# Kernel tuning notes

Hardware: AMD Instinct MI355X
Metric: run time of the kernel (lower is better)

The kernel has to match this reference:

```python
import jax, jax.numpy as jnp
import numpy as np

HEADS = 4
DIM_HEAD = 32


def setup_inputs() -> dict:
    key = jax.random.key(0)
    k1, k2, k3, k4 = jax.random.split(key, 4)
    x = jax.random.normal(k1, (2, 64, 48, 48, 48), dtype=jnp.float32)
    # 1x1x1 conv weights collapse to plain channel-mixing matrices
    w_qkv = jax.random.normal(k2, (384, 64), dtype=jnp.float32) * 0.05  # [3*heads*dh, dim]
    w_out = jax.random.normal(k3, (64, 128), dtype=jnp.float32) * 0.05  # [dim, heads*dh]
    b_out = jax.random.normal(k4, (64,), dtype=jnp.float32) * 0.05
    return {"x": x, "w_qkv": w_qkv, "w_out": w_out, "b_out": b_out}


def reference(x, w_qkv, w_out, b_out):
    b, c, D, H, W = x.shape
    N = D * H * W
    x_flat = x.reshape(b, c, N)
    # 1x1 conv == channel matmul: [b, 3*heads*dh, N]
    qkv = jnp.einsum('oc,bcn->bon', w_qkv, x_flat)
    # channel order: (qkv, heads, dh)
    qkv = qkv.reshape(b, 3, HEADS, DIM_HEAD, N)
    q, k, v = qkv[:, 0], qkv[:, 1], qkv[:, 2]
    k = jax.nn.softmax(k, axis=-1)  # softmax over the token axis N
    context = jnp.einsum('bhdn,bhen->bhde', k, v)   # [b, h, dh, dh]
    out = jnp.einsum('bhde,bhdn->bhen', context, q)  # [b, h, dh, N]
    out = out.reshape(b, HEADS * DIM_HEAD, N)
    y = jnp.einsum('oc,bcn->bon', w_out, out) + b_out[None, :, None]
    return y.reshape(b, c, D, H, W)
```

## Files before the change

### kernel.cpp

```cpp
#include <hip/hip_runtime.h>


#define C_IN 64

typedef __attribute__((ext_vector_type(8))) short short8;
typedef __attribute__((ext_vector_type(4))) float f32x4;

static __device__ __forceinline__ unsigned short f2bf(float f) {
    union { float f; unsigned u; } x; x.f = f;
    return (unsigned short)((x.u + 0x7fffu + ((x.u >> 16) & 1u)) >> 16);
}

__global__ __launch_bounds__(256, 3)
void kv_ctx_fused(const float* __restrict__ x,
                  const float* __restrict__ w_qkv,
                  unsigned short* __restrict__ xT,
                  float* __restrict__ part,
                  int N, int nblk, int bbase)
{
    __shared__ __align__(16) unsigned short Xsb[64][68];
    __shared__ __align__(16) unsigned short Xbf[64][72];
    __shared__ __align__(16) unsigned short PVs[4 * 2 * 32 * 64];

    const int by  = blockIdx.y;
    const int b   = by + bbase;
    const int bx  = blockIdx.x;
    const int t   = threadIdx.x;
    const int w   = t >> 6;
    const int l   = t & 63;
    const int l15 = l & 15;
    const int lg  = l >> 4;

    const float* xb = x + (size_t)b * C_IN * N;
    const int n_blk = bx * 256;

    auto pv_ptr = [&](int wp, int row, int colbf) -> unsigned short* {
        int byte = ((wp * 32 + row) << 7) + (((colbf << 1)) ^ ((row & 7) << 4));
        return (unsigned short*)((char*)PVs + byte);
    };

    short8 Wf[4][2];
    #pragma unroll
    for (int nt = 0; nt < 4; ++nt) {
        const int row = (nt < 2) ? (128 + w * 32 + nt * 16 + l15)
                                 : (256 + w * 32 + (nt - 2) * 16 + l15);
        const float* wr = w_qkv + (size_t)row * C_IN;
        #pragma unroll
        for (int s = 0; s < 2; ++s) {
            #pragma unroll
            for (int j = 0; j < 8; ++j)
                Wf[nt][s][j] = (short)f2bf(wr[s * 32 + lg * 8 + j]);
        }
    }

    f32x4 acc2[2][2];
    #pragma unroll
    for (int dt = 0; dt < 2; ++dt)
        #pragma unroll
        for (int et = 0; et < 2; ++et)
            acc2[dt][et] = (f32x4){0.f, 0.f, 0.f, 0.f};
    float s_loc[2] = {0.f, 0.f};

    float4 ld0, ld1, ld2, ld3;

    #define ISSUE_LOADS(IT) {                                              \
        const int nb2 = n_blk + (IT) * 64;                                 \
        int slot, c, nq;                                                   \
        slot = 0 * 256 + t; c = slot >> 4; nq = slot & 15;                 \
        ld0 = *(const float4*)(xb + (size_t)c * N + nb2 + nq * 4);         \
        slot = 1 * 256 + t; c = slot >> 4; nq = slot & 15;                 \
        ld1 = *(const float4*)(xb + (size_t)c * N + nb2 + nq * 4);         \
        slot = 2 * 256 + t; c = slot >> 4; nq = slot & 15;                 \
        ld2 = *(const float4*)(xb + (size_t)c * N + nb2 + nq * 4);         \
        slot = 3 * 256 + t; c = slot >> 4; nq = slot & 15;                 \
        ld3 = *(const float4*)(xb + (size_t)c * N + nb2 + nq * 4);         \
    }
    #define STORE_XSB() {                                                  \
        float4 lds_[4] = {ld0, ld1, ld2, ld3};                             \
        _Pragma("unroll")                                                  \
        for (int i = 0; i < 4; ++i) {                                      \
            int slot = i * 256 + t;                                        \
            int c = slot >> 4, n4 = (slot & 15) * 4;                       \
            uint2 p;                                                       \
            p.x = (unsigned)f2bf(lds_[i].x) | ((unsigned)f2bf(lds_[i].y) << 16); \
            p.y = (unsigned)f2bf(lds_[i].z) | ((unsigned)f2bf(lds_[i].w) << 16); \
            *(uint2*)&Xsb[c][n4] = p;                                      \
        }                                                                  \
    }

    ISSUE_LOADS(0)
    STORE_XSB()
    __syncthreads();

    for (int it = 0; it < 4; ++it) {
        if (it < 3) ISSUE_LOADS(it + 1)

        {
            const int an = l;
            unsigned rowu[8];
            #pragma unroll
            for (int i = 0; i < 8; ++i) {
                unsigned lo = Xsb[w * 16 + 2 * i][an];
                unsigned hi = Xsb[w * 16 + 2 * i + 1][an];
                rowu[i] = lo | (hi << 16);
            }
            *(uint4*)&Xbf[an][w * 16]     = *(uint4*)&rowu[0];
            *(uint4*)&Xbf[an][w * 16 + 8] = *(uint4*)&rowu[4];
            unsigned short* dst = xT + ((size_t)by * N + n_blk + it * 64 + an) * 64 + w * 16;
            *(uint4*)(dst)     = *(uint4*)&rowu[0];
            *(uint4*)(dst + 8) = *(uint4*)&rowu[4];
        }
        __syncthreads();

        short8 Af[4][2];
        #pragma unroll
        for (int mt = 0; mt < 4; ++mt)
            #pragma unroll
            for (int s = 0; s < 2; ++s)
                Af[mt][s] = *(const short8*)&Xbf[mt * 16 + l15][s * 32 + lg * 8];

        #pragma unroll
        for (int mt = 0; mt < 4; ++mt) {
            #pragma unroll
            for (int nt = 0; nt < 4; ++nt) {
                f32x4 a = (f32x4){0.f, 0.f, 0.f, 0.f};
                a = __builtin_amdgcn_mfma_f32_16x16x32_bf16(Af[mt][0], Wf[nt][0], a, 0, 0, 0);
                a = __builtin_amdgcn_mfma_f32_16x16x32_bf16(Af[mt][1], Wf[nt][1], a, 0, 0, 0);
                const int nl = mt * 16 + lg * 4;
                if (nt < 2) {
                    float e0 = __expf(a[0]), e1 = __expf(a[1]);
                    float e2 = __expf(a[2]), e3 = __expf(a[3]);
                    s_loc[nt] += (e0 + e1) + (e2 + e3);
                    uint2 p;
                    p.x = (unsigned)f2bf(e0) | ((unsigned)f2bf(e1) << 16);
                    p.y = (unsigned)f2bf(e2) | ((unsigned)f2bf(e3) << 16);
                    *(uint2*)pv_ptr(w * 2, (nt & 1) * 16 + l15, nl) = p;
                } else {
                    uint2 p;
                    p.x = (unsigned)f2bf(a[0]) | ((unsigned)f2bf(a[1]) << 16);
                    p.y = (unsigned)f2bf(a[2]) | ((unsigned)f2bf(a[3]) << 16);
                    *(uint2*)pv_ptr(w * 2 + 1, (nt - 2) * 16 + l15, nl) = p;
                }
            }
        }

        #pragma unroll
        for (int ns = 0; ns < 2; ++ns) {
            short8 A2[2], B2[2];
            #pragma unroll
            for (int dt = 0; dt < 2; ++dt)
                A2[dt] = *(const short8*)pv_ptr(w * 2, dt * 16 + l15, ns * 32 + lg * 8);
            #pragma unroll
            for (int et = 0; et < 2; ++et)
                B2[et] = *(const short8*)pv_ptr(w * 2 + 1, et * 16 + l15, ns * 32 + lg * 8);
            #pragma unroll
            for (int dt = 0; dt < 2; ++dt)
                #pragma unroll
                for (int et = 0; et < 2; ++et)
                    acc2[dt][et] = __builtin_amdgcn_mfma_f32_16x16x32_bf16(
                        A2[dt], B2[et], acc2[dt][et], 0, 0, 0);
        }

        if (it < 3) STORE_XSB()
        __syncthreads();
    }
    #undef ISSUE_LOADS
    #undef STORE_XSB

    float* pb = part + ((size_t)b * nblk + bx) * 4224;
    #pragma unroll
    for (int dt = 0; dt < 2; ++dt)
        #pragma unroll
        for (int et = 0; et < 2; ++et)
            #pragma unroll
            for (int r = 0; r < 4; ++r)
                pb[(w * 32 + dt * 16 + lg * 4 + r) * 32 + et * 16 + l15] =
                    acc2[dt][et][r];

    #pragma unroll
    for (int nt = 0; nt < 2; ++nt) {
        float s = s_loc[nt];
        s += __shfl_xor(s, 16);
        s += __shfl_xor(s, 32);
        if (lg == 0)
            pb[4096 + w * 32 + nt * 16 + l15] = s;
    }
}

__global__ __launch_bounds__(256)
void reduce_kernel(const float* __restrict__ part,
                   float* __restrict__ part2,
                   int nblk)
{
    const int b  = blockIdx.z;
    const int cy = blockIdx.y;
    const int g  = blockIdx.x * 256 + threadIdx.x;
    if (g >= 4224) return;

    const int cnt = (nblk + 15) / 16;
    const int c0  = cy * cnt;
    const int c1  = (c0 + cnt < nblk) ? (c0 + cnt) : nblk;

    const float* pb = part + (size_t)b * nblk * 4224 + g;
    float a0 = 0.f, a1 = 0.f, a2 = 0.f, a3 = 0.f;
    int c = c0;
    for (; c + 4 <= c1; c += 4) {
        a0 += pb[(size_t)(c + 0) * 4224];
        a1 += pb[(size_t)(c + 1) * 4224];
        a2 += pb[(size_t)(c + 2) * 4224];
        a3 += pb[(size_t)(c + 3) * 4224];
    }
    for (; c < c1; ++c) a0 += pb[(size_t)c * 4224];
    part2[((size_t)b * 16 + cy) * 4224 + g] = (a0 + a1) + (a2 + a3);
}

__global__ __launch_bounds__(256)
void finalize_kernel(const float* __restrict__ part2,
                     const float* __restrict__ w_qkv,
                     const float* __restrict__ w_out,
                     unsigned short* __restrict__ wf_bf)
{
    const int b = blockIdx.y;
    const int s = blockIdx.x;
    const int t = threadIdx.x;

    __shared__ float Wq[128][64];
    __shared__ float Ctx[128][36];
    __shared__ float Tt[128][68];
    __shared__ float WoS[8][128];
    __shared__ float Sinv[128];

    #pragma unroll
    for (int i = 0; i < 8; ++i) {
        int idx = i * 1024 + t * 4;
        *(float4*)&Wq[idx >> 6][idx & 63] = *(const float4*)(w_qkv + idx);
    }
    {
        int idx = t * 4;
        int o = idx >> 7, he = idx & 127;
        *(float4*)&WoS[o][he] = *(const float4*)(w_out + (size_t)(s * 8 + o) * 128 + he);
    }
    if (t < 128) {
        float ssum = 0.f;
        #pragma unroll
        for (int rep = 0; rep < 16; ++rep)
            ssum += part2[((size_t)b * 16 + rep) * 4224 + 4096 + t];
        Sinv[t] = 1.0f / ssum;
    }
    float cacc[16];
    #pragma unroll
    for (int i = 0; i < 16; ++i) cacc[i] = 0.f;
    {
        const float* cb = part2 + (size_t)b * 16 * 4224;
        for (int rep = 0; rep < 16; ++rep) {
            #pragma unroll
            for (int i = 0; i < 16; ++i)
                cacc[i] += cb[(size_t)rep * 4224 + i * 256 + t];
        }
    }
    __syncthreads();

    #pragma unroll
    for (int i = 0; i < 16; ++i) {
        int idx = i * 256 + t;
        Ctx[idx >> 5][idx & 31] = cacc[i] * Sinv[idx >> 5];
    }
    __syncthreads();

    {
        const int he0 = (t >> 3) * 4;
        const int c0  = (t & 7) * 8;
        const int hh  = he0 >> 5;
        const int e0  = he0 & 31;
        float acc[4][8];
        #pragma unroll
        for (int j = 0; j < 4; ++j)
            #pragma unroll
            for (int k = 0; k < 8; ++k) acc[j][k] = 0.f;

        for (int d = 0; d < 32; ++d) {
            float4 cv = *(const float4*)&Ctx[hh * 32 + d][e0];
            float4 w0 = *(const float4*)&Wq[hh * 32 + d][c0];
            float4 w1 = *(const float4*)&Wq[hh * 32 + d][c0 + 4];
            float wv[8] = {w0.x, w0.y, w0.z, w0.w, w1.x, w1.y, w1.z, w1.w};
            float cvv[4] = {cv.x, cv.y, cv.z, cv.w};
            #pragma unroll
            for (int j = 0; j < 4; ++j)
                #pragma unroll
                for (int k = 0; k < 8; ++k)
                    acc[j][k] = fmaf(cvv[j], wv[k], acc[j][k]);
        }
        #pragma unroll
        for (int j = 0; j < 4; ++j) {
            *(float4*)&Tt[he0 + j][c0]     = make_float4(acc[j][0], acc[j][1], acc[j][2], acc[j][3]);
            *(float4*)&Tt[he0 + j][c0 + 4] = make_float4(acc[j][4], acc[j][5], acc[j][6], acc[j][7]);
        }
    }
    __syncthreads();

    {
        const int o = t >> 5;
        const int c = (t & 31) * 2;
        float a0 = 0.f, a1 = 0.f, b0 = 0.f, b1 = 0.f;
        #pragma unroll
        for (int he = 0; he < 128; he += 2) {
            float w0 = WoS[o][he], w1 = WoS[o][he + 1];
            float2 t0 = *(const float2*)&Tt[he][c];
            float2 t1 = *(const float2*)&Tt[he + 1][c];
            a0 = fmaf(w0, t0.x, a0); a1 = fmaf(w0, t0.y, a1);
            b0 = fmaf(w1, t1.x, b0); b1 = fmaf(w1, t1.y, b1);
        }
        unsigned short* dst = wf_bf + (size_t)b * 4096 + (size_t)(s * 8 + o) * 64 + c;
        dst[0] = f2bf(a0 + b0);
        dst[1] = f2bf(a1 + b1);
    }
}

__global__ __launch_bounds__(256)
void out_gemm_mfma(const unsigned short* __restrict__ xT,
                   const unsigned short* __restrict__ wf_bf,
                   const float* __restrict__ b_out,
                   float* __restrict__ y,
                   int N, int bbase)
{
    const int by  = blockIdx.y;
    const int b   = by + bbase;
    const int t   = threadIdx.x;
    const int w   = t >> 6;
    const int l   = t & 63;
    const int l15 = l & 15;
    const int lg  = l >> 4;
    const int nb  = blockIdx.x * 256 + w * 64;

    short8 Bf[4][2];
    const unsigned short* wb = wf_bf + (size_t)b * 4096;
    #pragma unroll
    for (int ot = 0; ot < 4; ++ot)
        #pragma unroll
        for (int s = 0; s < 2; ++s)
            Bf[ot][s] = *(const short8*)(wb + (size_t)(ot * 16 + l15) * 64
                                         + s * 32 + lg * 8);
    float bias[4];
    #pragma unroll
    for (int ot = 0; ot < 4; ++ot) bias[ot] = b_out[ot * 16 + l15];

    short8 Af[4][2];
    const unsigned short* xr = xT + ((size_t)by * N + nb) * 64;
    #pragma unroll
    for (int mt = 0; mt < 4; ++mt)
        #pragma unroll
        for (int s = 0; s < 2; ++s)
            Af[mt][s] = *(const short8*)(xr + (size_t)(mt * 16 + l15) * 64
                                         + s * 32 + lg * 8);

    float* yb = y + (size_t)b * C_IN * N;
    #pragma unroll
    for (int mt = 0; mt < 4; ++mt) {
        #pragma unroll
        for (int ot = 0; ot < 4; ++ot) {
            f32x4 a = (f32x4){0.f, 0.f, 0.f, 0.f};
            a = __builtin_amdgcn_mfma_f32_16x16x32_bf16(Af[mt][0], Bf[ot][0], a, 0, 0, 0);
            a = __builtin_amdgcn_mfma_f32_16x16x32_bf16(Af[mt][1], Bf[ot][1], a, 0, 0, 0);
            float4 v = make_float4(a[0] + bias[ot], a[1] + bias[ot],
                                   a[2] + bias[ot], a[3] + bias[ot]);
            *(float4*)(yb + (size_t)(ot * 16 + l15) * N + nb + mt * 16 + lg * 4) = v;
        }
    }
}

__global__ __launch_bounds__(256)
void transpose_kernel(const float* __restrict__ x,
                      unsigned short* __restrict__ xT,
                      int N, int bbase)
{
    __shared__ float Xs[64][65];
    const int b  = blockIdx.y + bbase;
    const int t  = threadIdx.x;
    const int n0 = blockIdx.x * 64;

    const float* xb = x + (size_t)b * C_IN * N;
    #pragma unroll
    for (int i = 0; i < 4; ++i) {
        int slot = i * 256 + t;
        int c = slot >> 4, nq = slot & 15;
        float4 v = *(const float4*)(xb + (size_t)c * N + n0 + nq * 4);
        Xs[c][nq * 4 + 0] = v.x; Xs[c][nq * 4 + 1] = v.y;
        Xs[c][nq * 4 + 2] = v.z; Xs[c][nq * 4 + 3] = v.w;
    }
    __syncthreads();

    const int n = t >> 2, q = t & 3;
    unsigned out[8];
    #pragma unroll
    for (int i = 0; i < 8; ++i) {
        float lo = Xs[q * 16 + 2 * i][n], hi = Xs[q * 16 + 2 * i + 1][n];
        out[i] = (unsigned)f2bf(lo) | ((unsigned)f2bf(hi) << 16);
    }
    unsigned short* dst = xT + ((size_t)blockIdx.y * N + n0 + n) * 64 + q * 16;
    *(uint4*)(dst)     = *(uint4*)&out[0];
    *(uint4*)(dst + 8) = *(uint4*)&out[4];
}

extern "C" void kernel_launch(void* const* d_in, const int* in_sizes, int n_in,
                              void* d_out, int out_size, void* d_ws, size_t ws_size,
                              hipStream_t stream)
{
    const float* x     = (const float*)d_in[0];
    const float* w_qkv = (const float*)d_in[1];
    const float* w_out = (const float*)d_in[2];
    const float* b_out = (const float*)d_in[3];
    float* y = (float*)d_out;

    const int B = 2;
    const int N = in_sizes[0] / (B * C_IN);
    const int nblk = N / 256;

    const size_t xT_batch = (size_t)N * 64 * 2;
    const size_t part_b   = (size_t)B * nblk * 4224 * 4;
    const size_t p2_b     = (size_t)B * 16 * 4224 * 4;
    const size_t wf_b     = (size_t)B * 4096 * 2;
    const bool   full     = ws_size >= (size_t)B * xT_batch + part_b + p2_b + wf_b;

    unsigned short* xT    = (unsigned short*)d_ws;
    char* p               = (char*)d_ws + (full ? B * xT_batch : xT_batch);
    float* part           = (float*)p;
    float* part2          = part + (size_t)B * nblk * 4224;
    unsigned short* wf_bf = (unsigned short*)(part2 + (size_t)B * 16 * 4224);

    if (full) {
        kv_ctx_fused<<<dim3(nblk, B), 256, 0, stream>>>(x, w_qkv, xT, part, N, nblk, 0);
        reduce_kernel<<<dim3(17, 16, B), 256, 0, stream>>>(part, part2, nblk);
        finalize_kernel<<<dim3(8, B), 256, 0, stream>>>(part2, w_qkv, w_out, wf_bf);
        out_gemm_mfma<<<dim3(nblk, B), 256, 0, stream>>>(xT, wf_bf, b_out, y, N, 0);
    } else {
        for (int b = 0; b < B; ++b)
            kv_ctx_fused<<<dim3(nblk, 1), 256, 0, stream>>>(x, w_qkv, xT, part, N, nblk, b);
        reduce_kernel<<<dim3(17, 16, B), 256, 0, stream>>>(part, part2, nblk);
        finalize_kernel<<<dim3(8, B), 256, 0, stream>>>(part2, w_qkv, w_out, wf_bf);
        for (int b = 0; b < B; ++b) {
            transpose_kernel<<<dim3(N / 64, 1), 256, 0, stream>>>(x, xT, N, b);
            out_gemm_mfma<<<dim3(nblk, 1), 256, 0, stream>>>(xT, wf_bf, b_out, y, N, b);
        }
    }
}
```

Before: 67.40 us.

## Fuse four kernels into one cooperative persistent kernel with grid syncs

Replaces the four-kernel pipeline (kv context, reduce, finalize, output GEMM) with a single cooperative kernel. Each block processes two 256-token units, and grid.sync separates the phases. This removes launch gaps and tail effects between the kernels. In exchange it adds three grid-wide barriers, idles most blocks during the small reduce and finalize phases, and relies on co-residency of 432 blocks. It falls back to the old multi-kernel path if cooperative launch is unavailable, and the low-workspace per-batch fallback is removed.

Result: no change. 67.59 us (+0.3%).

```diff
diff --git a/kernel.cpp b/kernel.cpp
--- a/kernel.cpp
+++ b/kernel.cpp
@@ -1,4 +1,7 @@
 #include <hip/hip_runtime.h>
+#include <hip/hip_cooperative_groups.h>
+
+namespace cg = cooperative_groups;
 
 
 #define C_IN 64
@@ -9,6 +12,352 @@
 static __device__ __forceinline__ unsigned short f2bf(float f) {
     union { float f; unsigned u; } x; x.f = f;
     return (unsigned short)((x.u + 0x7fffu + ((x.u >> 16) & 1u)) >> 16);
+}
+
+__global__ __launch_bounds__(256, 3)
+void mega_kernel(const float* __restrict__ x,
+                 const float* __restrict__ w_qkv,
+                 const float* __restrict__ w_out,
+                 const float* __restrict__ b_out,
+                 unsigned short* __restrict__ xT,
+                 float* __restrict__ part,
+                 float* __restrict__ part2,
+                 unsigned short* __restrict__ wf_bf,
+                 float* __restrict__ y,
+                 int N, int nblk)
+{
+    cg::grid_group grid = cg::this_grid();
+    __shared__ __align__(16) char smem[53248];
+
+    const int bid = blockIdx.x;
+    const int t   = threadIdx.x;
+    const int w   = t >> 6;
+    const int l   = t & 63;
+    const int l15 = l & 15;
+    const int lg  = l >> 4;
+
+    unsigned short (*Xsb)[68] = (unsigned short (*)[68])smem;
+    unsigned short (*Xbf)[72] = (unsigned short (*)[72])(smem + 8704);
+    char* PVs = smem + 8704 + 9216;
+
+    auto pv_ptr = [&](int wp, int row, int colbf) -> unsigned short* {
+        int byte = ((wp * 32 + row) << 7) + ((colbf << 1) ^ ((row & 7) << 4));
+        return (unsigned short*)(PVs + byte);
+    };
+
+    {
+        short8 Wfr[4][2];
+        #pragma unroll
+        for (int nt = 0; nt < 4; ++nt) {
+            const int row = (nt < 2) ? (128 + w * 32 + nt * 16 + l15)
+                                     : (256 + w * 32 + (nt - 2) * 16 + l15);
+            const float* wr = w_qkv + (size_t)row * C_IN;
+            #pragma unroll
+            for (int s = 0; s < 2; ++s) {
+                #pragma unroll
+                for (int j = 0; j < 8; ++j)
+                    Wfr[nt][s][j] = (short)f2bf(wr[s * 32 + lg * 8 + j]);
+            }
+        }
+
+        for (int u2 = 0; u2 < 2; ++u2) {
+            const int unit = bid * 2 + u2;
+            const int b = unit / nblk, jc = unit - b * nblk;
+            const float* xb = x + (size_t)b * C_IN * N;
+            const int n_blk = jc * 256;
+
+            f32x4 acc2[2][2];
+            #pragma unroll
+            for (int dt = 0; dt < 2; ++dt)
+                #pragma unroll
+                for (int et = 0; et < 2; ++et)
+                    acc2[dt][et] = (f32x4){0.f, 0.f, 0.f, 0.f};
+            float s_loc[2] = {0.f, 0.f};
+
+            float4 ld0, ld1, ld2, ld3;
+
+            #define ISSUE_LOADS(IT) {                                          \
+                const int nb2 = n_blk + (IT) * 64;                             \
+                int slot, c, nq;                                               \
+                slot = 0 * 256 + t; c = slot >> 4; nq = slot & 15;             \
+                ld0 = *(const float4*)(xb + (size_t)c * N + nb2 + nq * 4);     \
+                slot = 1 * 256 + t; c = slot >> 4; nq = slot & 15;             \
+                ld1 = *(const float4*)(xb + (size_t)c * N + nb2 + nq * 4);     \
+                slot = 2 * 256 + t; c = slot >> 4; nq = slot & 15;             \
+                ld2 = *(const float4*)(xb + (size_t)c * N + nb2 + nq * 4);     \
+                slot = 3 * 256 + t; c = slot >> 4; nq = slot & 15;             \
+                ld3 = *(const float4*)(xb + (size_t)c * N + nb2 + nq * 4);     \
+            }
+            #define STORE_XSB() {                                              \
+                float4 lds_[4] = {ld0, ld1, ld2, ld3};                         \
+                _Pragma("unroll")                                              \
+                for (int i = 0; i < 4; ++i) {                                  \
+                    int slot = i * 256 + t;                                    \
+                    int c = slot >> 4, n4 = (slot & 15) * 4;                   \
+                    uint2 p;                                                   \
+                    p.x = (unsigned)f2bf(lds_[i].x) | ((unsigned)f2bf(lds_[i].y) << 16); \
+                    p.y = (unsigned)f2bf(lds_[i].z) | ((unsigned)f2bf(lds_[i].w) << 16); \
+                    *(uint2*)&Xsb[c][n4] = p;                                  \
+                }                                                              \
+            }
+
+            ISSUE_LOADS(0)
+            STORE_XSB()
+            __syncthreads();
+
+            for (int it = 0; it < 4; ++it) {
+                if (it < 3) ISSUE_LOADS(it + 1)
+
+                {
+                    const int an = l;
+                    unsigned rowu[8];
+                    #pragma unroll
+                    for (int i = 0; i < 8; ++i) {
+                        unsigned lo = Xsb[w * 16 + 2 * i][an];
+                        unsigned hi = Xsb[w * 16 + 2 * i + 1][an];
+                        rowu[i] = lo | (hi << 16);
+                    }
+                    *(uint4*)&Xbf[an][w * 16]     = *(uint4*)&rowu[0];
+                    *(uint4*)&Xbf[an][w * 16 + 8] = *(uint4*)&rowu[4];
+                    unsigned short* dst = xT + ((size_t)b * N + n_blk + it * 64 + an) * 64 + w * 16;
+                    *(uint4*)(dst)     = *(uint4*)&rowu[0];
+                    *(uint4*)(dst + 8) = *(uint4*)&rowu[4];
+                }
+                __syncthreads();
+
+                short8 Af[4][2];
+                #pragma unroll
+                for (int mt = 0; mt < 4; ++mt)
+                    #pragma unroll
+                    for (int s = 0; s < 2; ++s)
+                        Af[mt][s] = *(const short8*)&Xbf[mt * 16 + l15][s * 32 + lg * 8];
+
+                #pragma unroll
+                for (int mt = 0; mt < 4; ++mt) {
+                    #pragma unroll
+                    for (int nt = 0; nt < 4; ++nt) {
+                        f32x4 a = (f32x4){0.f, 0.f, 0.f, 0.f};
+                        a = __builtin_amdgcn_mfma_f32_16x16x32_bf16(Af[mt][0], Wfr[nt][0], a, 0, 0, 0);
+                        a = __builtin_amdgcn_mfma_f32_16x16x32_bf16(Af[mt][1], Wfr[nt][1], a, 0, 0, 0);
+                        const int nl = mt * 16 + lg * 4;
+                        if (nt < 2) {
+                            float e0 = __expf(a[0]), e1 = __expf(a[1]);
+                            float e2 = __expf(a[2]), e3 = __expf(a[3]);
+                            s_loc[nt] += (e0 + e1) + (e2 + e3);
+                            uint2 p;
+                            p.x = (unsigned)f2bf(e0) | ((unsigned)f2bf(e1) << 16);
+                            p.y = (unsigned)f2bf(e2) | ((unsigned)f2bf(e3) << 16);
+                            *(uint2*)pv_ptr(w * 2, (nt & 1) * 16 + l15, nl) = p;
+                        } else {
+                            uint2 p;
+                            p.x = (unsigned)f2bf(a[0]) | ((unsigned)f2bf(a[1]) << 16);
+                            p.y = (unsigned)f2bf(a[2]) | ((unsigned)f2bf(a[3]) << 16);
+                            *(uint2*)pv_ptr(w * 2 + 1, (nt - 2) * 16 + l15, nl) = p;
+                        }
+                    }
+                }
+
+                #pragma unroll
+                for (int ns = 0; ns < 2; ++ns) {
+                    short8 A2[2], B2[2];
+                    #pragma unroll
+                    for (int dt = 0; dt < 2; ++dt)
+                        A2[dt] = *(const short8*)pv_ptr(w * 2, dt * 16 + l15, ns * 32 + lg * 8);
+                    #pragma unroll
+                    for (int et = 0; et < 2; ++et)
+                        B2[et] = *(const short8*)pv_ptr(w * 2 + 1, et * 16 + l15, ns * 32 + lg * 8);
+                    #pragma unroll
+                    for (int dt = 0; dt < 2; ++dt)
+                        #pragma unroll
+                        for (int et = 0; et < 2; ++et)
+                            acc2[dt][et] = __builtin_amdgcn_mfma_f32_16x16x32_bf16(
+                                A2[dt], B2[et], acc2[dt][et], 0, 0, 0);
+                }
+
+                if (it < 3) STORE_XSB()
+                __syncthreads();
+            }
+            #undef ISSUE_LOADS
+            #undef STORE_XSB
+
+            float* pb = part + (size_t)unit * 4224;
+            #pragma unroll
+            for (int dt = 0; dt < 2; ++dt)
+                #pragma unroll
+                for (int et = 0; et < 2; ++et)
+                    #pragma unroll
+                    for (int r = 0; r < 4; ++r)
+                        pb[(w * 32 + dt * 16 + lg * 4 + r) * 32 + et * 16 + l15] =
+                            acc2[dt][et][r];
+
+            #pragma unroll
+            for (int nt = 0; nt < 2; ++nt) {
+                float s = s_loc[nt];
+                s += __shfl_xor(s, 16);
+                s += __shfl_xor(s, 32);
+                if (lg == 0)
+                    pb[4096 + w * 32 + nt * 16 + l15] = s;
+            }
+        }
+    }
+    __threadfence();
+    grid.sync();
+
+    if (bid < 17 * 16) {
+        const int gy  = bid >> 4;
+        const int rep = bid & 15;
+        const int g   = gy * 256 + t;
+        if (g < 4224) {
+            const int cnt = nblk / 16;
+            #pragma unroll
+            for (int b = 0; b < 2; ++b) {
+                const float* pb = part + ((size_t)b * nblk + rep * cnt) * 4224 + g;
+                float a0 = 0.f, a1 = 0.f, a2 = 0.f, a3 = 0.f;
+                int c = 0;
+                for (; c + 4 <= cnt; c += 4) {
+                    a0 += pb[(size_t)(c + 0) * 4224];
+                    a1 += pb[(size_t)(c + 1) * 4224];
+                    a2 += pb[(size_t)(c + 2) * 4224];
+                    a3 += pb[(size_t)(c + 3) * 4224];
+                }
+                for (; c < cnt; ++c) a0 += pb[(size_t)c * 4224];
+                part2[((size_t)b * 16 + rep) * 4224 + g] = (a0 + a1) + (a2 + a3);
+            }
+        }
+    }
+    __threadfence();
+    grid.sync();
+
+    if (bid < 16) {
+        const int b = bid >> 3, s = bid & 7;
+        float (*Ctx)[36] = (float (*)[36])smem;
+        float (*Tt)[68]  = (float (*)[68])(smem + 18432);
+
+        if (t < 128) {
+            float ssum = 0.f;
+            #pragma unroll
+            for (int rep = 0; rep < 16; ++rep)
+                ssum += part2[((size_t)b * 16 + rep) * 4224 + 4096 + t];
+            Ctx[t][32] = 1.0f / ssum;
+        }
+        float cacc[16];
+        #pragma unroll
+        for (int i = 0; i < 16; ++i) cacc[i] = 0.f;
+        {
+            const float* cb = part2 + (size_t)b * 16 * 4224;
+            for (int rep = 0; rep < 16; ++rep) {
+                #pragma unroll
+                for (int i = 0; i < 16; ++i)
+                    cacc[i] += cb[(size_t)rep * 4224 + i * 256 + t];
+            }
+        }
+        __syncthreads();
+
+        #pragma unroll
+        for (int i = 0; i < 16; ++i) {
+            int idx = i * 256 + t;
+            int hd = idx >> 5, e = idx & 31;
+            Ctx[hd][e] = cacc[i] * Ctx[hd][32];
+        }
+        __syncthreads();
+
+        {
+            const int he0 = (t >> 3) * 4;
+            const int c0  = (t & 7) * 8;
+            const int hh  = he0 >> 5;
+            const int e0  = he0 & 31;
+            float acc[4][8];
+            #pragma unroll
+            for (int j = 0; j < 4; ++j)
+                #pragma unroll
+                for (int k = 0; k < 8; ++k) acc[j][k] = 0.f;
+
+            const float* wqb = w_qkv + (size_t)(hh * 32) * C_IN + c0;
+            #pragma unroll 4
+            for (int d = 0; d < 32; ++d) {
+                float4 cv = *(const float4*)&Ctx[hh * 32 + d][e0];
+                float4 w0 = *(const float4*)(wqb + (size_t)d * C_IN);
+                float4 w1 = *(const float4*)(wqb + (size_t)d * C_IN + 4);
+                float wv[8] = {w0.x, w0.y, w0.z, w0.w, w1.x, w1.y, w1.z, w1.w};
+                float cvv[4] = {cv.x, cv.y, cv.z, cv.w};
+                #pragma unroll
+                for (int j = 0; j < 4; ++j)
+                    #pragma unroll
+                    for (int k = 0; k < 8; ++k)
+                        acc[j][k] = fmaf(cvv[j], wv[k], acc[j][k]);
+            }
+            #pragma unroll
+            for (int j = 0; j < 4; ++j) {
+                *(float4*)&Tt[he0 + j][c0]     = make_float4(acc[j][0], acc[j][1], acc[j][2], acc[j][3]);
+                *(float4*)&Tt[he0 + j][c0 + 4] = make_float4(acc[j][4], acc[j][5], acc[j][6], acc[j][7]);
+            }
+        }
+        __syncthreads();
+
+        {
+            const int o = t >> 5;
+            const int c = (t & 31) * 2;
+            const float* wo = w_out + (size_t)(s * 8 + o) * 128;
+            float a0 = 0.f, a1 = 0.f, b0 = 0.f, b1 = 0.f;
+            #pragma unroll 4
+            for (int he = 0; he < 128; he += 2) {
+                float w0 = wo[he], w1 = wo[he + 1];
+                float2 t0 = *(const float2*)&Tt[he][c];
+                float2 t1 = *(const float2*)&Tt[he + 1][c];
+                a0 = fmaf(w0, t0.x, a0); a1 = fmaf(w0, t0.y, a1);
+                b0 = fmaf(w1, t1.x, b0); b1 = fmaf(w1, t1.y, b1);
+            }
+            unsigned short* dst = wf_bf + (size_t)b * 4096 + (size_t)(s * 8 + o) * 64 + c;
+            dst[0] = f2bf(a0 + b0);
+            dst[1] = f2bf(a1 + b1);
+        }
+    }
+    __threadfence();
+    grid.sync();
+
+    {
+        float bias[4];
+        #pragma unroll
+        for (int ot = 0; ot < 4; ++ot) bias[ot] = b_out[ot * 16 + l15];
+
+        for (int u2 = 0; u2 < 2; ++u2) {
+            const int unit = bid * 2 + u2;
+            const int b = unit / nblk, jc = unit - b * nblk;
+            const int nb = jc * 256 + w * 64;
+
+            short8 Bf2[4][2];
+            const unsigned short* wb = wf_bf + (size_t)b * 4096;
+            #pragma unroll
+            for (int ot = 0; ot < 4; ++ot)
+                #pragma unroll
+                for (int s = 0; s < 2; ++s)
+                    Bf2[ot][s] = *(const short8*)(wb + (size_t)(ot * 16 + l15) * 64
+                                                  + s * 32 + lg * 8);
+
+            short8 Af2[4][2];
+            const unsigned short* xr = xT + ((size_t)b * N + nb) * 64;
+            #pragma unroll
+            for (int mt = 0; mt < 4; ++mt)
+                #pragma unroll
+                for (int s = 0; s < 2; ++s)
+                    Af2[mt][s] = *(const short8*)(xr + (size_t)(mt * 16 + l15) * 64
+                                                  + s * 32 + lg * 8);
+
+            float* yb = y + (size_t)b * C_IN * N;
+            #pragma unroll
+            for (int mt = 0; mt < 4; ++mt) {
+                #pragma unroll
+                for (int ot = 0; ot < 4; ++ot) {
+                    f32x4 a = (f32x4){0.f, 0.f, 0.f, 0.f};
+                    a = __builtin_amdgcn_mfma_f32_16x16x32_bf16(Af2[mt][0], Bf2[ot][0], a, 0, 0, 0);
+                    a = __builtin_amdgcn_mfma_f32_16x16x32_bf16(Af2[mt][1], Bf2[ot][1], a, 0, 0, 0);
+                    float4 v = make_float4(a[0] + bias[ot], a[1] + bias[ot],
+                                           a[2] + bias[ot], a[3] + bias[ot]);
+                    *(float4*)(yb + (size_t)(ot * 16 + l15) * N + nb + mt * 16 + lg * 4) = v;
+                }
+            }
+        }
+    }
 }
 
 __global__ __launch_bounds__(256, 3)
@@ -35,11 +384,11 @@
     const int n_blk = bx * 256;
 
     auto pv_ptr = [&](int wp, int row, int colbf) -> unsigned short* {
-        int byte = ((wp * 32 + row) << 7) + (((colbf << 1)) ^ ((row & 7) << 4));
+        int byte = ((wp * 32 + row) << 7) + ((colbf << 1) ^ ((row & 7) << 4));
         return (unsigned short*)((char*)PVs + byte);
     };
 
-    short8 Wf[4][2];
+    short8 Wfr[4][2];
     #pragma unroll
     for (int nt = 0; nt < 4; ++nt) {
         const int row = (nt < 2) ? (128 + w * 32 + nt * 16 + l15)
@@ -49,7 +398,7 @@
         for (int s = 0; s < 2; ++s) {
             #pragma unroll
             for (int j = 0; j < 8; ++j)
-                Wf[nt][s][j] = (short)f2bf(wr[s * 32 + lg * 8 + j]);
+                Wfr[nt][s][j] = (short)f2bf(wr[s * 32 + lg * 8 + j]);
         }
     }
 
@@ -124,8 +473,8 @@
             #pragma unroll
             for (int nt = 0; nt < 4; ++nt) {
                 f32x4 a = (f32x4){0.f, 0.f, 0.f, 0.f};
-                a = __builtin_amdgcn_mfma_f32_16x16x32_bf16(Af[mt][0], Wf[nt][0], a, 0, 0, 0);
-                a = __builtin_amdgcn_mfma_f32_16x16x32_bf16(Af[mt][1], Wf[nt][1], a, 0, 0, 0);
+                a = __builtin_amdgcn_mfma_f32_16x16x32_bf16(Af[mt][0], Wfr[nt][0], a, 0, 0, 0);
+                a = __builtin_amdgcn_mfma_f32_16x16x32_bf16(Af[mt][1], Wfr[nt][1], a, 0, 0, 0);
                 const int nl = mt * 16 + lg * 4;
                 if (nt < 2) {
                     float e0 = __expf(a[0]), e1 = __expf(a[1]);
@@ -368,39 +717,6 @@
     }
 }
 
-__global__ __launch_bounds__(256)
-void transpose_kernel(const float* __restrict__ x,
-                      unsigned short* __restrict__ xT,
-                      int N, int bbase)
-{
-    __shared__ float Xs[64][65];
-    const int b  = blockIdx.y + bbase;
-    const int t  = threadIdx.x;
-    const int n0 = blockIdx.x * 64;
-
-    const float* xb = x + (size_t)b * C_IN * N;
-    #pragma unroll
-    for (int i = 0; i < 4; ++i) {
-        int slot = i * 256 + t;
-        int c = slot >> 4, nq = slot & 15;
-        float4 v = *(const float4*)(xb + (size_t)c * N + n0 + nq * 4);
-        Xs[c][nq * 4 + 0] = v.x; Xs[c][nq * 4 + 1] = v.y;
-        Xs[c][nq * 4 + 2] = v.z; Xs[c][nq * 4 + 3] = v.w;
-    }
-    __syncthreads();
-
-    const int n = t >> 2, q = t & 3;
-    unsigned out[8];
-    #pragma unroll
-    for (int i = 0; i < 8; ++i) {
-        float lo = Xs[q * 16 + 2 * i][n], hi = Xs[q * 16 + 2 * i + 1][n];
-        out[i] = (unsigned)f2bf(lo) | ((unsigned)f2bf(hi) << 16);
-    }
-    unsigned short* dst = xT + ((size_t)blockIdx.y * N + n0 + n) * 64 + q * 16;
-    *(uint4*)(dst)     = *(uint4*)&out[0];
-    *(uint4*)(dst + 8) = *(uint4*)&out[4];
-}
-
 extern "C" void kernel_launch(void* const* d_in, const int* in_sizes, int n_in,
                               void* d_out, int out_size, void* d_ws, size_t ws_size,
                               hipStream_t stream)
@@ -414,32 +730,47 @@
     const int B = 2;
     const int N = in_sizes[0] / (B * C_IN);
     const int nblk = N / 256;
-
-    const size_t xT_batch = (size_t)N * 64 * 2;
-    const size_t part_b   = (size_t)B * nblk * 4224 * 4;
-    const size_t p2_b     = (size_t)B * 16 * 4224 * 4;
-    const size_t wf_b     = (size_t)B * 4096 * 2;
-    const bool   full     = ws_size >= (size_t)B * xT_batch + part_b + p2_b + wf_b;
+    const int total_units = B * nblk;
+
+    const size_t xT_b   = (size_t)B * N * 64 * 2;
+    const size_t part_b = (size_t)total_units * 4224 * 4;
+    const size_t p2_b   = (size_t)B * 16 * 4224 * 4;
+    const size_t wf_b   = (size_t)B * 4096 * 2;
+    const bool   fits   = ws_size >= xT_b + part_b + p2_b + wf_b;
 
     unsigned short* xT    = (unsigned short*)d_ws;
-    char* p               = (char*)d_ws + (full ? B * xT_batch : xT_batch);
-    float* part           = (float*)p;
-    float* part2          = part + (size_t)B * nblk * 4224;
+    float* part           = (float*)((char*)d_ws + xT_b);
+    float* part2          = part + (size_t)total_units * 4224;
     unsigned short* wf_bf = (unsigned short*)(part2 + (size_t)B * 16 * 4224);
 
-    if (full) {
+    bool coop_done = false;
+    if (fits && (nblk % 16 == 0) && (total_units % 2 == 0)) {
+        const int G = total_units / 2;
+        int dev = 0, cus = 0, maxb = 0;
+        bool ok = (hipGetDevice(&dev) == hipSuccess);
+        ok = ok && (hipDeviceGetAttribute(&cus,
+                        hipDeviceAttributeMultiprocessorCount, dev) == hipSuccess);
+        ok = ok && (hipOccupancyMaxActiveBlocksPerMultiprocessor(&maxb,
+                        mega_kernel, 256, 0) == hipSuccess);
+        if (ok && (long)maxb * cus >= G && G >= 17 * 16) {
+            const float* xa = x; const float* wqa = w_qkv;
+            const float* woa = w_out; const float* boa = b_out;
+            unsigned short* xTa = xT; float* pa = part; float* p2a = part2;
+            unsigned short* wfa = wf_bf; float* ya = y;
+            int Na = N, nblka = nblk;
+            void* args[] = {&xa, &wqa, &woa, &boa, &xTa, &pa, &p2a, &wfa, &ya,
+                            &Na, &nblka};
+            hipError_t e = hipLaunchCooperativeKernel((void*)mega_kernel,
+                                                      dim3(G), dim3(256),
+                                                      args, 0, stream);
+            coop_done = (e == hipSuccess);
+        }
+    }
+
+    if (!coop_done) {
         kv_ctx_fused<<<dim3(nblk, B), 256, 0, stream>>>(x, w_qkv, xT, part, N, nblk, 0);
         reduce_kernel<<<dim3(17, 16, B), 256, 0, stream>>>(part, part2, nblk);
         finalize_kernel<<<dim3(8, B), 256, 0, stream>>>(part2, w_qkv, w_out, wf_bf);
         out_gemm_mfma<<<dim3(nblk, B), 256, 0, stream>>>(xT, wf_bf, b_out, y, N, 0);
-    } else {
-        for (int b = 0; b < B; ++b)
-            kv_ctx_fused<<<dim3(nblk, 1), 256, 0, stream>>>(x, w_qkv, xT, part, N, nblk, b);
-        reduce_kernel<<<dim3(17, 16, B), 256, 0, stream>>>(part, part2, nblk);
-        finalize_kernel<<<dim3(8, B), 256, 0, stream>>>(part2, w_qkv, w_out, wf_bf);
-        for (int b = 0; b < B; ++b) {
-            transpose_kernel<<<dim3(N / 64, 1), 256, 0, stream>>>(x, xT, N, b);
-            out_gemm_mfma<<<dim3(nblk, 1), 256, 0, stream>>>(xT, wf_bf, b_out, y, N, b);
-        }
     }
 }
```

## Halve per-wave P/V LDS staging to fit four blocks per CU

Applied to the files above, without the earlier changes.

The QKV projection and context accumulation now run over two 32-token halves per 64-token tile instead of the full 64 tokens at once. This shrinks the per-wave P/V staging buffer, and the XOR swizzle is replaced with padded 80-byte rows. The smaller LDS footprint lets launch bounds rise from 3 to 4 blocks per CU, aiming for better latency hiding on the bandwidth-heavy x read. In exchange, the tighter register budget may cause spills, and the padded layout may bring back some LDS bank conflicts.

Result: slower. 88.11 us (+30.7%).

```diff
diff --git a/kernel.cpp b/kernel.cpp
--- a/kernel.cpp
+++ b/kernel.cpp
@@ -11,7 +11,7 @@
     return (unsigned short)((x.u + 0x7fffu + ((x.u >> 16) & 1u)) >> 16);
 }
 
-__global__ __launch_bounds__(256, 3)
+__global__ __launch_bounds__(256, 4)
 void kv_ctx_fused(const float* __restrict__ x,
                   const float* __restrict__ w_qkv,
                   unsigned short* __restrict__ xT,
@@ -20,7 +20,7 @@
 {
     __shared__ __align__(16) unsigned short Xsb[64][68];
     __shared__ __align__(16) unsigned short Xbf[64][72];
-    __shared__ __align__(16) unsigned short PVs[4 * 2 * 32 * 64];
+    __shared__ __align__(16) char PVs[4 * 2 * 32 * 80];
 
     const int by  = blockIdx.y;
     const int b   = by + bbase;
@@ -34,12 +34,12 @@
     const float* xb = x + (size_t)b * C_IN * N;
     const int n_blk = bx * 256;
 
-    auto pv_ptr = [&](int wp, int row, int colbf) -> unsigned short* {
-        int byte = ((wp * 32 + row) << 7) + (((colbf << 1)) ^ ((row & 7) << 4));
-        return (unsigned short*)((char*)PVs + byte);
+    auto pv_ptr = [&](int p, int row, int colbf) -> unsigned short* {
+        return (unsigned short*)(PVs + ((size_t)((w * 2 + p) * 32 + row) * 80
+                                        + colbf * 2));
     };
 
-    short8 Wf[4][2];
+    short8 Wfr[4][2];
     #pragma unroll
     for (int nt = 0; nt < 4; ++nt) {
         const int row = (nt < 2) ? (128 + w * 32 + nt * 16 + l15)
@@ -49,7 +49,7 @@
         for (int s = 0; s < 2; ++s) {
             #pragma unroll
             for (int j = 0; j < 8; ++j)
-                Wf[nt][s][j] = (short)f2bf(wr[s * 32 + lg * 8 + j]);
+                Wfr[nt][s][j] = (short)f2bf(wr[s * 32 + lg * 8 + j]);
         }
     }
 
@@ -120,45 +120,47 @@
                 Af[mt][s] = *(const short8*)&Xbf[mt * 16 + l15][s * 32 + lg * 8];
 
         #pragma unroll
-        for (int mt = 0; mt < 4; ++mt) {
-            #pragma unroll
-            for (int nt = 0; nt < 4; ++nt) {
-                f32x4 a = (f32x4){0.f, 0.f, 0.f, 0.f};
-                a = __builtin_amdgcn_mfma_f32_16x16x32_bf16(Af[mt][0], Wf[nt][0], a, 0, 0, 0);
-                a = __builtin_amdgcn_mfma_f32_16x16x32_bf16(Af[mt][1], Wf[nt][1], a, 0, 0, 0);
-                const int nl = mt * 16 + lg * 4;
-                if (nt < 2) {
-                    float e0 = __expf(a[0]), e1 = __expf(a[1]);
-                    float e2 = __expf(a[2]), e3 = __expf(a[3]);
-                    s_loc[nt] += (e0 + e1) + (e2 + e3);
-                    uint2 p;
-                    p.x = (unsigned)f2bf(e0) | ((unsigned)f2bf(e1) << 16);
-                    p.y = (unsigned)f2bf(e2) | ((unsigned)f2bf(e3) << 16);
-                    *(uint2*)pv_ptr(w * 2, (nt & 1) * 16 + l15, nl) = p;
-                } else {
-                    uint2 p;
-                    p.x = (unsigned)f2bf(a[0]) | ((unsigned)f2bf(a[1]) << 16);
-                    p.y = (unsigned)f2bf(a[2]) | ((unsigned)f2bf(a[3]) << 16);
-                    *(uint2*)pv_ptr(w * 2 + 1, (nt - 2) * 16 + l15, nl) = p;
+        for (int h = 0; h < 2; ++h) {
+            #pragma unroll
+            for (int m2 = 0; m2 < 2; ++m2) {
+                const int mt = h * 2 + m2;
+                #pragma unroll
+                for (int nt = 0; nt < 4; ++nt) {
+                    f32x4 a = (f32x4){0.f, 0.f, 0.f, 0.f};
+                    a = __builtin_amdgcn_mfma_f32_16x16x32_bf16(Af[mt][0], Wfr[nt][0], a, 0, 0, 0);
+                    a = __builtin_amdgcn_mfma_f32_16x16x32_bf16(Af[mt][1], Wfr[nt][1], a, 0, 0, 0);
+                    const int nh = m2 * 16 + lg * 4;
+                    if (nt < 2) {
+                        float e0 = __expf(a[0]), e1 = __expf(a[1]);
+                        float e2 = __expf(a[2]), e3 = __expf(a[3]);
+                        s_loc[nt] += (e0 + e1) + (e2 + e3);
+                        uint2 p;
+                        p.x = (unsigned)f2bf(e0) | ((unsigned)f2bf(e1) << 16);
+                        p.y = (unsigned)f2bf(e2) | ((unsigned)f2bf(e3) << 16);
+                        *(uint2*)pv_ptr(0, nt * 16 + l15, nh) = p;
+                    } else {
+                        uint2 p;
+                        p.x = (unsigned)f2bf(a[0]) | ((unsigned)f2bf(a[1]) << 16);
+                        p.y = (unsigned)f2bf(a[2]) | ((unsigned)f2bf(a[3]) << 16);
+                        *(uint2*)pv_ptr(1, (nt - 2) * 16 + l15, nh) = p;
+                    }
                 }
             }
-        }
-
-        #pragma unroll
-        for (int ns = 0; ns < 2; ++ns) {
-            short8 A2[2], B2[2];
-            #pragma unroll
-            for (int dt = 0; dt < 2; ++dt)
-                A2[dt] = *(const short8*)pv_ptr(w * 2, dt * 16 + l15, ns * 32 + lg * 8);
-            #pragma unroll
-            for (int et = 0; et < 2; ++et)
-                B2[et] = *(const short8*)pv_ptr(w * 2 + 1, et * 16 + l15, ns * 32 + lg * 8);
-            #pragma unroll
-            for (int dt = 0; dt < 2; ++dt)
+            {
+                short8 A2[2], B2[2];
+                #pragma unroll
+                for (int dt = 0; dt < 2; ++dt)
+                    A2[dt] = *(const short8*)pv_ptr(0, dt * 16 + l15, lg * 8);
                 #pragma unroll
                 for (int et = 0; et < 2; ++et)
-                    acc2[dt][et] = __builtin_amdgcn_mfma_f32_16x16x32_bf16(
-                        A2[dt], B2[et], acc2[dt][et], 0, 0, 0);
+                    B2[et] = *(const short8*)pv_ptr(1, et * 16 + l15, lg * 8);
+                #pragma unroll
+                for (int dt = 0; dt < 2; ++dt)
+                    #pragma unroll
+                    for (int et = 0; et < 2; ++et)
+                        acc2[dt][et] = __builtin_amdgcn_mfma_f32_16x16x32_bf16(
+                            A2[dt], B2[et], acc2[dt][et], 0, 0, 0);
+            }
         }
 
         if (it < 3) STORE_XSB()
```
